# Performance work log

Hardware: AMD Instinct MI355X
Metric: run time of the kernel (lower is better)

## Reference

```python
import jax, jax.numpy as jnp
import numpy as np

B, C, T = 16, 256, 2048          # bsz, z_dim (fsz), tsz
PRED_STEPS, N_NEG, OFFSET = 12, 15, 16
COPIES = 1 + N_NEG


def setup_inputs() -> dict:
    key = jax.random.key(0)
    k1, k2, k3 = jax.random.split(key, 3)
    z = jax.random.normal(k1, (B, C, T), jnp.float32)
    # ConvTranspose2d(C, C, (1, PRED_STEPS)) weight, size-1 kernel-height dim dropped
    weight = jax.random.normal(k2, (C, C, PRED_STEPS), jnp.float32) * 0.02
    bias = jnp.zeros((C,), jnp.float32)
    # negative index sampling (done under no_grad in the original):
    # tszs[k] = k // N_NEG, r in [0, B*T-1), bump by 1 where r >= t
    tszs = jnp.repeat(jnp.arange(T, dtype=jnp.int32), N_NEG)   # (N_NEG*T,)
    r = jax.random.randint(k3, (B, N_NEG * T), 0, B * T - 1, dtype=jnp.int32)
    neg_idxs = r + (r >= tszs[None, :]).astype(jnp.int32)      # values in [0, B*T)
    return {"z": z, "weight": weight, "bias": bias, "neg_idxs": neg_idxs}


def reference(z, weight, bias, neg_idxs):
    # encoder / aggregator are identity: z_hat = z
    # predictor: pred_steps independent linear maps of z_hat
    z_pred = jnp.einsum('bct,coi->boti', z, weight) + bias[None, :, None, None]  # (B,C,T,S)

    # --- sample_negatives: gather from flattened (C, B*T) bank ---
    y = jnp.transpose(z, (1, 0, 2)).reshape(C, B * T)           # (C, B*T)
    negs = y[:, neg_idxs.reshape(-1)]                           # (C, B*N_NEG*T)
    negs = negs.reshape(C, B, N_NEG, T)
    negs = jnp.transpose(negs, (2, 1, 0, 3))                    # (N_NEG, B, C, T)

    targets = jnp.concatenate([z[None], negs], axis=0)          # (COPIES, B, C, T)

    steps = min(PRED_STEPS, T - OFFSET)
    preds = []
    for i in range(steps):  # fixed small structural loop (12 steps)
        off = i + OFFSET
        # ('bct,nbct->tbn') on the overlapping slices, written flat
        p = jnp.einsum('bct,nbct->tbn', z_pred[:, :, :T - off, i], targets[..., off:])
        preds.append(p.reshape(-1))
    predictions = jnp.concatenate(preds).reshape(-1, COPIES)
    labels = jnp.zeros((predictions.shape[0],), dtype=jnp.int32)
    return predictions, labels
```

## Files before the change

### kernel.cpp

```cpp
#include <hip/hip_runtime.h>
#include <hip/hip_bf16.h>

#define B_   16
#define C_   256
#define T_   2048
#define PS   12
#define NNEG 15
#define OFFS 16
#define COPIES 16

#define M_GEMM (B_ * T_)
#define N_GEMM (C_ * PS)
#define K_GEMM C_
#define NPRED 6225408
#define NLAB  389088

using bf16 = __hip_bfloat16;
typedef __attribute__((ext_vector_type(4))) float f32x4;
typedef __attribute__((ext_vector_type(8))) short bf16x8;

__global__ __launch_bounds__(256) void transpose_z(const float* __restrict__ z,
                                                   bf16* __restrict__ zT) {
    __shared__ float tile[32][33];
    int t0 = blockIdx.x * 32, c0 = blockIdx.y * 32, b = blockIdx.z;
    int col = threadIdx.x & 31, r = threadIdx.x >> 5;
    for (int rr = 0; rr < 4; ++rr) {
        int row = r + rr * 8;
        tile[row][col] = z[(size_t)(b * C_ + c0 + row) * T_ + t0 + col];
    }
    __syncthreads();
    for (int rr = 0; rr < 4; ++rr) {
        int row = r + rr * 8;
        zT[(size_t)(b * T_ + t0 + row) * C_ + c0 + col] =
            __float2bfloat16(tile[col][row]);
    }
}

__global__ __launch_bounds__(256) void pack_w(const float* __restrict__ w,
                                              bf16* __restrict__ wTb) {
    int gid = blockIdx.x * 256 + threadIdx.x;
    int j = gid >> 8, c = gid & 255;
    int o = j & 255, i = j >> 8;
    wTb[gid] = __float2bfloat16(w[(size_t)c * (C_ * PS) + o * PS + i]);
}

#define BM 128
#define BN 128
#define BK 64
#define EPAD 136

__global__ __launch_bounds__(256) void gemm_zpred(const bf16* __restrict__ zT,
                                                  const bf16* __restrict__ wTb,
                                                  const float* __restrict__ bias,
                                                  bf16* __restrict__ zp) {
    __shared__ __align__(16) char smem[BM * EPAD * 2];
    bf16* lA = (bf16*)smem;
    bf16* lB = (bf16*)(smem + 16384);
    bf16* lE = (bf16*)smem;

    int bid = (blockIdx.x & 7) * 768 + (blockIdx.x >> 3);
    int bn = bid % (N_GEMM / BN);
    int bm = bid / (N_GEMM / BN);
    int tid = threadIdx.x;
    int wid = tid >> 6, lane = tid & 63;
    int ln15 = lane & 15, kg = lane >> 4;
    int wm = (wid & 1) * 64, wn = (wid >> 1) * 64;
    int row0 = bm * BM, col0 = bn * BN;
    int i_step = col0 >> 8;
    int o0 = col0 & 255;

    f32x4 acc[4][4] = {};

    int rsw = (((lane & 7) ^ ((lane >> 3) & 7)) * 8);
    int srow = wid * 8 + (lane >> 3);
    const bf16* gA0 = zT + (size_t)(row0 + srow) * 256 + rsw;
    const bf16* gB0 = wTb + (size_t)(col0 + srow) * 256 + rsw;

#pragma unroll
    for (int kt = 0; kt < K_GEMM / BK; ++kt) {
        if (kt) __syncthreads();
#pragma unroll
        for (int it = 0; it < 4; ++it) {
            __builtin_amdgcn_global_load_lds(
                (const __attribute__((address_space(1))) void*)(gA0 + it * (size_t)(32 * 256) + kt * BK),
                (__attribute__((address_space(3))) void*)(smem + it * 4096 + wid * 1024), 16, 0, 0);
            __builtin_amdgcn_global_load_lds(
                (const __attribute__((address_space(1))) void*)(gB0 + it * (size_t)(32 * 256) + kt * BK),
                (__attribute__((address_space(3))) void*)(smem + 16384 + it * 4096 + wid * 1024), 16, 0, 0);
        }
        __syncthreads();

#pragma unroll
        for (int kk = 0; kk < 2; ++kk) {
            bf16x8 af[4], bfr[4];
#pragma unroll
            for (int mi = 0; mi < 4; ++mi) {
                int row = wm + mi * 16 + ln15;
                int g = (kk * 4 + kg) ^ (ln15 & 7);
                af[mi] = *(const bf16x8*)&lA[row * BK + g * 8];
            }
#pragma unroll
            for (int ni = 0; ni < 4; ++ni) {
                int row = wn + ni * 16 + ln15;
                int g = (kk * 4 + kg) ^ (ln15 & 7);
                bfr[ni] = *(const bf16x8*)&lB[row * BK + g * 8];
            }
#pragma unroll
            for (int mi = 0; mi < 4; ++mi)
#pragma unroll
                for (int ni = 0; ni < 4; ++ni)
                    acc[mi][ni] = __builtin_amdgcn_mfma_f32_16x16x32_bf16(
                        af[mi], bfr[ni], acc[mi][ni], 0, 0, 0);
        }
    }

    __syncthreads();

    float bv[4];
#pragma unroll
    for (int ni = 0; ni < 4; ++ni) bv[ni] = bias[o0 + wn + ni * 16 + ln15];

#pragma unroll
    for (int mi = 0; mi < 4; ++mi)
#pragma unroll
        for (int ni = 0; ni < 4; ++ni) {
            int col_e = wn + ni * 16 + ln15;
#pragma unroll
            for (int r = 0; r < 4; ++r) {
                int row_e = wm + mi * 16 + kg * 4 + r;
                lE[row_e * EPAD + col_e] = __float2bfloat16(acc[mi][ni][r] + bv[ni]);
            }
        }

    __syncthreads();

#pragma unroll
    for (int e = 0; e < 8; ++e) {
        int row_e = e * 16 + (tid >> 4);
        int grow = row0 + row_e;
        int b = grow >> 11, t = grow & (T_ - 1);
        int s = t + OFFS + i_step;
        if (s < T_) {
            bf16x8 v = *(const bf16x8*)&lE[row_e * EPAD + (tid & 15) * 8];
            *(bf16x8*)(zp + ((size_t)(b * T_ + s) * PS + i_step) * 256 + o0 +
                       (tid & 15) * 8) = v;
        }
    }
}

__global__ __launch_bounds__(256) void predict_kernel(
    const bf16* __restrict__ zT, const bf16* __restrict__ zp,
    const int* __restrict__ neg, float* __restrict__ out) {
    int tid = threadIdx.x;
    int wid = tid >> 6, lane = tid & 63;
    int ln15 = lane & 15, kg = lane >> 4;
    int gw = blockIdx.x * 4 + wid;
    int b = gw / (T_ - OFFS);
    int s = OFFS + gw % (T_ - OFFS);

    int src;
    if (ln15 == 0) src = b * T_ + s;
    else           src = neg[b * (NNEG * T_) + (ln15 - 1) * T_ + s];
    const bf16* arow = zT + (size_t)src * 256 + kg * 8;
    const bf16* brow = zp + ((size_t)(b * T_ + s) * PS + ln15) * 256 + kg * 8;

    f32x4 acc = {0.f, 0.f, 0.f, 0.f};
#pragma unroll
    for (int kk = 0; kk < 8; ++kk) {
        bf16x8 a = *(const bf16x8*)(arow + kk * 32);
        bf16x8 bb = *(const bf16x8*)(brow + kk * 32);
        acc = __builtin_amdgcn_mfma_f32_16x16x32_bf16(a, bb, acc, 0, 0, 0);
    }

    int i = ln15;
    int imax = s - OFFS; if (imax > PS - 1) imax = PS - 1;
    if (i <= imax) {
        int t = s - OFFS - i;
        int base_i = 256 * ((T_ - OFFS) * i - (i * (i - 1)) / 2);
        float* o = out + base_i + (t * B_ + b) * COPIES + kg * 4;
        o[0] = acc[0]; o[1] = acc[1]; o[2] = acc[2]; o[3] = acc[3];
    }
}

extern "C" void kernel_launch(void* const* d_in, const int* in_sizes, int n_in,
                              void* d_out, int out_size, void* d_ws, size_t ws_size,
                              hipStream_t stream) {
    const float* z    = (const float*)d_in[0];
    const float* w    = (const float*)d_in[1];
    const float* bias = (const float*)d_in[2];
    const int*   neg  = (const int*)d_in[3];
    float* out = (float*)d_out;

    char* ws = (char*)d_ws;
    const size_t ZP_BYTES = (size_t)B_ * T_ * PS * 256 * sizeof(bf16);
    bf16* zp  = (bf16*)ws;
    bf16* zT  = (bf16*)(ws + ZP_BYTES + 8192);
    bf16* wTb = (bf16*)(ws + ZP_BYTES + 8192 + (size_t)M_GEMM * 256 * sizeof(bf16));

    transpose_z<<<dim3(T_ / 32, C_ / 32, B_), 256, 0, stream>>>(z, zT);
    pack_w<<<(N_GEMM * 256) / 256, 256, 0, stream>>>(w, wTb);
    gemm_zpred<<<(M_GEMM / BM) * (N_GEMM / BN), 256, 0, stream>>>(zT, wTb, bias, zp);
    predict_kernel<<<(B_ * (T_ - OFFS)) / 4, 256, 0, stream>>>(zT, zp, neg, out);
    hipMemsetAsync(out + NPRED, 0, NLAB * sizeof(float), stream);
}
```

Before: 166.4 us.

## Enlarge GEMM tile to 256x256 with 4-stage async LDS pipeline

```diff
diff --git a/kernel.cpp b/kernel.cpp
--- a/kernel.cpp
+++ b/kernel.cpp
@@ -18,6 +18,12 @@
 using bf16 = __hip_bfloat16;
 typedef __attribute__((ext_vector_type(4))) float f32x4;
 typedef __attribute__((ext_vector_type(8))) short bf16x8;
+
+#define WAITVM(n) asm volatile("s_waitcnt vmcnt(" #n ")" ::: "memory")
+#define GLL(src, dst)                                                        \
+    __builtin_amdgcn_global_load_lds(                                        \
+        (const __attribute__((address_space(1))) void*)(src),                \
+        (__attribute__((address_space(3))) void*)(dst), 16, 0, 0)
 
 __global__ __launch_bounds__(256) void transpose_z(const float* __restrict__ z,
                                                    bf16* __restrict__ zT) {
@@ -44,108 +50,131 @@
     wTb[gid] = __float2bfloat16(w[(size_t)c * (C_ * PS) + o * PS + i]);
 }
 
-#define BM 128
-#define BN 128
-#define BK 64
-#define EPAD 136
-
-__global__ __launch_bounds__(256) void gemm_zpred(const bf16* __restrict__ zT,
-                                                  const bf16* __restrict__ wTb,
-                                                  const float* __restrict__ bias,
-                                                  bf16* __restrict__ zp) {
-    __shared__ __align__(16) char smem[BM * EPAD * 2];
-    bf16* lA = (bf16*)smem;
-    bf16* lB = (bf16*)(smem + 16384);
+#define EPAD 264
+
+__global__ __launch_bounds__(512, 2) void gemm_zpred(
+    const bf16* __restrict__ zT, const bf16* __restrict__ wTb,
+    const float* __restrict__ bias, bf16* __restrict__ zp) {
+    __shared__ __align__(16) char smem[131072];
     bf16* lE = (bf16*)smem;
 
-    int bid = (blockIdx.x & 7) * 768 + (blockIdx.x >> 3);
-    int bn = bid % (N_GEMM / BN);
-    int bm = bid / (N_GEMM / BN);
+    int bid = (blockIdx.x & 7) * 192 + (blockIdx.x >> 3);
+    int bm = bid / (N_GEMM / 256);
+    int bn = bid % (N_GEMM / 256);
+    int row0 = bm * 256;
+    int col0 = bn * 256;
+
     int tid = threadIdx.x;
     int wid = tid >> 6, lane = tid & 63;
     int ln15 = lane & 15, kg = lane >> 4;
-    int wm = (wid & 1) * 64, wn = (wid >> 1) * 64;
-    int row0 = bm * BM, col0 = bn * BN;
-    int i_step = col0 >> 8;
-    int o0 = col0 & 255;
-
-    f32x4 acc[4][4] = {};
-
-    int rsw = (((lane & 7) ^ ((lane >> 3) & 7)) * 8);
-    int srow = wid * 8 + (lane >> 3);
-    const bf16* gA0 = zT + (size_t)(row0 + srow) * 256 + rsw;
-    const bf16* gB0 = wTb + (size_t)(col0 + srow) * 256 + rsw;
-
-#pragma unroll
-    for (int kt = 0; kt < K_GEMM / BK; ++kt) {
-        if (kt) __syncthreads();
-#pragma unroll
-        for (int it = 0; it < 4; ++it) {
-            __builtin_amdgcn_global_load_lds(
-                (const __attribute__((address_space(1))) void*)(gA0 + it * (size_t)(32 * 256) + kt * BK),
-                (__attribute__((address_space(3))) void*)(smem + it * 4096 + wid * 1024), 16, 0, 0);
-            __builtin_amdgcn_global_load_lds(
-                (const __attribute__((address_space(1))) void*)(gB0 + it * (size_t)(32 * 256) + kt * BK),
-                (__attribute__((address_space(3))) void*)(smem + 16384 + it * 4096 + wid * 1024), 16, 0, 0);
+    int wr = wid >> 2, wc = wid & 3;
+
+    int srow = wid * 16 + (lane >> 2);
+    int gsw = ((lane & 3) ^ ((srow >> 1) & 3)) * 8;
+    const bf16* srcA0 = zT + (size_t)(row0 + srow) * 256 + gsw;
+    const bf16* srcA1 = srcA0 + 128 * 256;
+    const bf16* srcB0 = wTb + (size_t)(col0 + srow) * 256 + gsw;
+    const bf16* srcB1 = srcB0 + 128 * 256;
+
+    int offA[8], offB[4];
+#pragma unroll
+    for (int mi = 0; mi < 8; ++mi) {
+        int rl = wr * 128 + mi * 16 + ln15;
+        offA[mi] = (rl >> 7) * 8192 + (rl & 127) * 64 +
+                   ((kg ^ ((rl >> 1) & 3)) * 16);
+    }
+#pragma unroll
+    for (int ni = 0; ni < 4; ++ni) {
+        int cl = wc * 64 + ni * 16 + ln15;
+        offB[ni] = (cl >> 7) * 8192 + (cl & 127) * 64 +
+                   ((kg ^ ((cl >> 1) & 3)) * 16);
+    }
+
+    f32x4 acc[8][4] = {};
+
+#define STAGE(t, slot)                                                       \
+    {                                                                        \
+        const bf16* a0 = srcA0 + (t) * 32;                                   \
+        const bf16* b0 = srcB0 + (t) * 32;                                   \
+        char* d = smem + (slot) * 32768 + wid * 1024;                        \
+        GLL(a0, d);                                                          \
+        GLL(srcA1 + (t) * 32, d + 8192);                                     \
+        GLL(b0, d + 16384);                                                  \
+        GLL(srcB1 + (t) * 32, d + 24576);                                    \
+    }
+
+#define TILE_ITER(KT, VM)                                                    \
+    {                                                                        \
+        WAITVM(VM);                                                          \
+        __builtin_amdgcn_s_barrier();                                        \
+        char* sb = smem + ((KT) & 3) * 32768;                                \
+        bf16x8 af[8], bfr[4];                                                \
+        _Pragma("unroll") for (int mi = 0; mi < 8; ++mi)                     \
+            af[mi] = *(const bf16x8*)(sb + offA[mi]);                        \
+        _Pragma("unroll") for (int ni = 0; ni < 4; ++ni)                     \
+            bfr[ni] = *(const bf16x8*)(sb + 16384 + offB[ni]);               \
+        asm volatile("s_waitcnt lgkmcnt(0)" ::: "memory");                   \
+        __builtin_amdgcn_sched_barrier(0);                                   \
+        __builtin_amdgcn_s_barrier();                                        \
+        if ((KT) + 4 < 8) STAGE((KT) + 4, (KT) & 3);                         \
+        __builtin_amdgcn_s_setprio(1);                                       \
+        _Pragma("unroll") for (int mi = 0; mi < 8; ++mi)                     \
+            _Pragma("unroll") for (int ni = 0; ni < 4; ++ni)                 \
+                acc[mi][ni] = __builtin_amdgcn_mfma_f32_16x16x32_bf16(       \
+                    af[mi], bfr[ni], acc[mi][ni], 0, 0, 0);                  \
+        __builtin_amdgcn_s_setprio(0);                                       \
+    }
+
+    STAGE(0, 0);
+    STAGE(1, 1);
+    STAGE(2, 2);
+    STAGE(3, 3);
+
+    TILE_ITER(0, 12);
+    TILE_ITER(1, 12);
+    TILE_ITER(2, 12);
+    TILE_ITER(3, 12);
+    TILE_ITER(4, 12);
+    TILE_ITER(5, 8);
+    TILE_ITER(6, 4);
+    TILE_ITER(7, 0);
+
+    float bv[4];
+#pragma unroll
+    for (int ni = 0; ni < 4; ++ni) bv[ni] = bias[wc * 64 + ni * 16 + ln15];
+
+    for (int h = 0; h < 2; ++h) {
+        __syncthreads();
+        if (wr == h) {
+#pragma unroll
+            for (int mi = 0; mi < 8; ++mi)
+#pragma unroll
+                for (int ni = 0; ni < 4; ++ni) {
+                    int cl = wc * 64 + ni * 16 + ln15;
+#pragma unroll
+                    for (int r = 0; r < 4; ++r) {
+                        int row_e = mi * 16 + kg * 4 + r;
+                        lE[row_e * EPAD + cl] =
+                            __float2bfloat16(acc[mi][ni][r] + bv[ni]);
+                    }
+                }
         }
         __syncthreads();
-
-#pragma unroll
-        for (int kk = 0; kk < 2; ++kk) {
-            bf16x8 af[4], bfr[4];
-#pragma unroll
-            for (int mi = 0; mi < 4; ++mi) {
-                int row = wm + mi * 16 + ln15;
-                int g = (kk * 4 + kg) ^ (ln15 & 7);
-                af[mi] = *(const bf16x8*)&lA[row * BK + g * 8];
-            }
-#pragma unroll
-            for (int ni = 0; ni < 4; ++ni) {
-                int row = wn + ni * 16 + ln15;
-                int g = (kk * 4 + kg) ^ (ln15 & 7);
-                bfr[ni] = *(const bf16x8*)&lB[row * BK + g * 8];
-            }
-#pragma unroll
-            for (int mi = 0; mi < 4; ++mi)
-#pragma unroll
-                for (int ni = 0; ni < 4; ++ni)
-                    acc[mi][ni] = __builtin_amdgcn_mfma_f32_16x16x32_bf16(
-                        af[mi], bfr[ni], acc[mi][ni], 0, 0, 0);
-        }
-    }
-
-    __syncthreads();
-
-    float bv[4];
-#pragma unroll
-    for (int ni = 0; ni < 4; ++ni) bv[ni] = bias[o0 + wn + ni * 16 + ln15];
-
-#pragma unroll
-    for (int mi = 0; mi < 4; ++mi)
-#pragma unroll
-        for (int ni = 0; ni < 4; ++ni) {
-            int col_e = wn + ni * 16 + ln15;
-#pragma unroll
-            for (int r = 0; r < 4; ++r) {
-                int row_e = wm + mi * 16 + kg * 4 + r;
-                lE[row_e * EPAD + col_e] = __float2bfloat16(acc[mi][ni][r] + bv[ni]);
+#pragma unroll
+        for (int e = 0; e < 8; ++e) {
+            int row_e = e * 16 + (tid >> 5);
+            int grow = row0 + h * 128 + row_e;
+            int b = grow >> 11, t = grow & (T_ - 1);
+            int s = t + OFFS + bn;
+            if (s < T_) {
+                bf16x8 v = *(const bf16x8*)&lE[row_e * EPAD + (tid & 31) * 8];
+                *(bf16x8*)(zp + ((size_t)(b * T_ + s) * PS + bn) * 256 +
+                           (tid & 31) * 8) = v;
             }
         }
-
-    __syncthreads();
-
-#pragma unroll
-    for (int e = 0; e < 8; ++e) {
-        int row_e = e * 16 + (tid >> 4);
-        int grow = row0 + row_e;
-        int b = grow >> 11, t = grow & (T_ - 1);
-        int s = t + OFFS + i_step;
-        if (s < T_) {
-            bf16x8 v = *(const bf16x8*)&lE[row_e * EPAD + (tid & 15) * 8];
-            *(bf16x8*)(zp + ((size_t)(b * T_ + s) * PS + i_step) * 256 + o0 +
-                       (tid & 15) * 8) = v;
-        }
-    }
+    }
+#undef STAGE
+#undef TILE_ITER
 }
 
 __global__ __launch_bounds__(256) void predict_kernel(
@@ -199,7 +228,7 @@
 
     transpose_z<<<dim3(T_ / 32, C_ / 32, B_), 256, 0, stream>>>(z, zT);
     pack_w<<<(N_GEMM * 256) / 256, 256, 0, stream>>>(w, wTb);
-    gemm_zpred<<<(M_GEMM / BM) * (N_GEMM / BN), 256, 0, stream>>>(zT, wTb, bias, zp);
+    gemm_zpred<<<(M_GEMM / 256) * (N_GEMM / 256), 512, 0, stream>>>(zT, wTb, bias, zp);
     predict_kernel<<<(B_ * (T_ - OFFS)) / 4, 256, 0, stream>>>(zT, zp, neg, out);
     hipMemsetAsync(out + NPRED, 0, NLAB * sizeof(float), stream);
 }
```

After: 181.1 us. 1.09x slower.

## Triple-buffer GEMM K-loop with async LDS loads and batch two positions per predict wave

Applied to the files above, without the earlier changes.

```diff
diff --git a/kernel.cpp b/kernel.cpp
--- a/kernel.cpp
+++ b/kernel.cpp
@@ -18,6 +18,12 @@
 using bf16 = __hip_bfloat16;
 typedef __attribute__((ext_vector_type(4))) float f32x4;
 typedef __attribute__((ext_vector_type(8))) short bf16x8;
+
+#define WAITVM(n) asm volatile("s_waitcnt vmcnt(" #n ")" ::: "memory")
+#define GLL(src, dst)                                                        \
+    __builtin_amdgcn_global_load_lds(                                        \
+        (const __attribute__((address_space(1))) void*)(src),                \
+        (__attribute__((address_space(3))) void*)(dst), 16, 0, 0)
 
 __global__ __launch_bounds__(256) void transpose_z(const float* __restrict__ z,
                                                    bf16* __restrict__ zT) {
@@ -44,75 +50,87 @@
     wTb[gid] = __float2bfloat16(w[(size_t)c * (C_ * PS) + o * PS + i]);
 }
 
-#define BM 128
-#define BN 128
-#define BK 64
 #define EPAD 136
 
 __global__ __launch_bounds__(256) void gemm_zpred(const bf16* __restrict__ zT,
                                                   const bf16* __restrict__ wTb,
                                                   const float* __restrict__ bias,
                                                   bf16* __restrict__ zp) {
-    __shared__ __align__(16) char smem[BM * EPAD * 2];
-    bf16* lA = (bf16*)smem;
-    bf16* lB = (bf16*)(smem + 16384);
+    __shared__ __align__(16) char smem[49152];
     bf16* lE = (bf16*)smem;
 
     int bid = (blockIdx.x & 7) * 768 + (blockIdx.x >> 3);
-    int bn = bid % (N_GEMM / BN);
-    int bm = bid / (N_GEMM / BN);
+    int bn = bid % (N_GEMM / 128);
+    int bm = bid / (N_GEMM / 128);
     int tid = threadIdx.x;
     int wid = tid >> 6, lane = tid & 63;
     int ln15 = lane & 15, kg = lane >> 4;
     int wm = (wid & 1) * 64, wn = (wid >> 1) * 64;
-    int row0 = bm * BM, col0 = bn * BN;
+    int row0 = bm * 128, col0 = bn * 128;
     int i_step = col0 >> 8;
     int o0 = col0 & 255;
 
+    int gsw = ((lane & 3) ^ ((lane >> 3) & 3)) * 8;
+    int srow = wid * 16 + (lane >> 2);
+    const bf16* srcA = zT + (size_t)(row0 + srow) * 256 + gsw;
+    const bf16* srcB = wTb + (size_t)(col0 + srow) * 256 + gsw;
+
+    int offA[4], offB[4];
+#pragma unroll
+    for (int mi = 0; mi < 4; ++mi) {
+        int r = wm + mi * 16 + ln15;
+        offA[mi] = r * 64 + ((kg ^ ((r >> 1) & 3)) * 16);
+    }
+#pragma unroll
+    for (int ni = 0; ni < 4; ++ni) {
+        int c = wn + ni * 16 + ln15;
+        offB[ni] = 8192 + c * 64 + ((kg ^ ((c >> 1) & 3)) * 16);
+    }
+
     f32x4 acc[4][4] = {};
 
-    int rsw = (((lane & 7) ^ ((lane >> 3) & 7)) * 8);
-    int srow = wid * 8 + (lane >> 3);
-    const bf16* gA0 = zT + (size_t)(row0 + srow) * 256 + rsw;
-    const bf16* gB0 = wTb + (size_t)(col0 + srow) * 256 + rsw;
-
-#pragma unroll
-    for (int kt = 0; kt < K_GEMM / BK; ++kt) {
-        if (kt) __syncthreads();
-#pragma unroll
-        for (int it = 0; it < 4; ++it) {
-            __builtin_amdgcn_global_load_lds(
-                (const __attribute__((address_space(1))) void*)(gA0 + it * (size_t)(32 * 256) + kt * BK),
-                (__attribute__((address_space(3))) void*)(smem + it * 4096 + wid * 1024), 16, 0, 0);
-            __builtin_amdgcn_global_load_lds(
-                (const __attribute__((address_space(1))) void*)(gB0 + it * (size_t)(32 * 256) + kt * BK),
-                (__attribute__((address_space(3))) void*)(smem + 16384 + it * 4096 + wid * 1024), 16, 0, 0);
-        }
-        __syncthreads();
-
-#pragma unroll
-        for (int kk = 0; kk < 2; ++kk) {
-            bf16x8 af[4], bfr[4];
-#pragma unroll
-            for (int mi = 0; mi < 4; ++mi) {
-                int row = wm + mi * 16 + ln15;
-                int g = (kk * 4 + kg) ^ (ln15 & 7);
-                af[mi] = *(const bf16x8*)&lA[row * BK + g * 8];
-            }
-#pragma unroll
-            for (int ni = 0; ni < 4; ++ni) {
-                int row = wn + ni * 16 + ln15;
-                int g = (kk * 4 + kg) ^ (ln15 & 7);
-                bfr[ni] = *(const bf16x8*)&lB[row * BK + g * 8];
-            }
-#pragma unroll
-            for (int mi = 0; mi < 4; ++mi)
-#pragma unroll
-                for (int ni = 0; ni < 4; ++ni)
-                    acc[mi][ni] = __builtin_amdgcn_mfma_f32_16x16x32_bf16(
-                        af[mi], bfr[ni], acc[mi][ni], 0, 0, 0);
-        }
-    }
+#define STAGE(t, slot_base)                                                  \
+    {                                                                        \
+        char* d = smem + (slot_base) + wid * 1024;                           \
+        const bf16* sa = srcA + (t) * 32;                                    \
+        const bf16* sb2 = srcB + (t) * 32;                                   \
+        GLL(sa, d);                                                          \
+        GLL(sa + 64 * 256, d + 4096);                                        \
+        GLL(sb2, d + 8192);                                                  \
+        GLL(sb2 + 64 * 256, d + 12288);                                      \
+    }
+
+#define TILE_BODY(slot_base, VMN)                                            \
+    {                                                                        \
+        WAITVM(VMN);                                                         \
+        __builtin_amdgcn_s_barrier();                                        \
+        const char* sb = smem + (slot_base);                                 \
+        bf16x8 af[4], bfr[4];                                                \
+        _Pragma("unroll") for (int mi = 0; mi < 4; ++mi)                     \
+            af[mi] = *(const bf16x8*)(sb + offA[mi]);                        \
+        _Pragma("unroll") for (int ni = 0; ni < 4; ++ni)                     \
+            bfr[ni] = *(const bf16x8*)(sb + offB[ni]);                       \
+        asm volatile("s_waitcnt lgkmcnt(0)" ::: "memory");                   \
+        __builtin_amdgcn_sched_barrier(0);                                   \
+        __builtin_amdgcn_s_barrier();                                        \
+        __builtin_amdgcn_s_setprio(1);                                       \
+        _Pragma("unroll") for (int mi = 0; mi < 4; ++mi)                     \
+            _Pragma("unroll") for (int ni = 0; ni < 4; ++ni)                 \
+                acc[mi][ni] = __builtin_amdgcn_mfma_f32_16x16x32_bf16(       \
+                    af[mi], bfr[ni], acc[mi][ni], 0, 0, 0);                  \
+        __builtin_amdgcn_s_setprio(0);                                       \
+    }
+
+    STAGE(0, 0);
+    STAGE(1, 16384);
+    STAGE(2, 32768);  TILE_BODY(0, 8);
+    STAGE(3, 0);      TILE_BODY(16384, 8);
+    STAGE(4, 16384);  TILE_BODY(32768, 8);
+    STAGE(5, 32768);  TILE_BODY(0, 8);
+    STAGE(6, 0);      TILE_BODY(16384, 8);
+    STAGE(7, 16384);  TILE_BODY(32768, 8);
+                      TILE_BODY(0, 4);
+                      TILE_BODY(16384, 0);
 
     __syncthreads();
 
@@ -146,6 +164,8 @@
                        (tid & 15) * 8) = v;
         }
     }
+#undef STAGE
+#undef TILE_BODY
 }
 
 __global__ __launch_bounds__(256) void predict_kernel(
@@ -154,31 +174,50 @@
     int tid = threadIdx.x;
     int wid = tid >> 6, lane = tid & 63;
     int ln15 = lane & 15, kg = lane >> 4;
-    int gw = blockIdx.x * 4 + wid;
+    int gw = (blockIdx.x * 4 + wid) * 2;
     int b = gw / (T_ - OFFS);
     int s = OFFS + gw % (T_ - OFFS);
 
-    int src;
-    if (ln15 == 0) src = b * T_ + s;
-    else           src = neg[b * (NNEG * T_) + (ln15 - 1) * T_ + s];
-    const bf16* arow = zT + (size_t)src * 256 + kg * 8;
-    const bf16* brow = zp + ((size_t)(b * T_ + s) * PS + ln15) * 256 + kg * 8;
-
-    f32x4 acc = {0.f, 0.f, 0.f, 0.f};
+    int src0, src1;
+    if (ln15 == 0) {
+        src0 = b * T_ + s;
+        src1 = src0 + 1;
+    } else {
+        const int* np = neg + b * (NNEG * T_) + (ln15 - 1) * T_ + s;
+        src0 = np[0];
+        src1 = np[1];
+    }
+    const bf16* a0 = zT + (size_t)src0 * 256 + kg * 8;
+    const bf16* a1 = zT + (size_t)src1 * 256 + kg * 8;
+    const bf16* b0 = zp + ((size_t)(b * T_ + s) * PS + ln15) * 256 + kg * 8;
+    const bf16* b1 = b0 + PS * 256;
+
+    f32x4 acc0 = {0.f, 0.f, 0.f, 0.f};
+    f32x4 acc1 = {0.f, 0.f, 0.f, 0.f};
 #pragma unroll
     for (int kk = 0; kk < 8; ++kk) {
-        bf16x8 a = *(const bf16x8*)(arow + kk * 32);
-        bf16x8 bb = *(const bf16x8*)(brow + kk * 32);
-        acc = __builtin_amdgcn_mfma_f32_16x16x32_bf16(a, bb, acc, 0, 0, 0);
+        bf16x8 av0 = *(const bf16x8*)(a0 + kk * 32);
+        bf16x8 bv0 = *(const bf16x8*)(b0 + kk * 32);
+        bf16x8 av1 = *(const bf16x8*)(a1 + kk * 32);
+        bf16x8 bv1 = *(const bf16x8*)(b1 + kk * 32);
+        acc0 = __builtin_amdgcn_mfma_f32_16x16x32_bf16(av0, bv0, acc0, 0, 0, 0);
+        acc1 = __builtin_amdgcn_mfma_f32_16x16x32_bf16(av1, bv1, acc1, 0, 0, 0);
     }
 
     int i = ln15;
-    int imax = s - OFFS; if (imax > PS - 1) imax = PS - 1;
-    if (i <= imax) {
-        int t = s - OFFS - i;
-        int base_i = 256 * ((T_ - OFFS) * i - (i * (i - 1)) / 2);
-        float* o = out + base_i + (t * B_ + b) * COPIES + kg * 4;
-        o[0] = acc[0]; o[1] = acc[1]; o[2] = acc[2]; o[3] = acc[3];
+    if (i < PS) {
+#pragma unroll 2
+        for (int p = 0; p < 2; ++p) {
+            int sp = s + p;
+            int imax = sp - OFFS;
+            if (i <= imax) {
+                int t = sp - OFFS - i;
+                int base_i = 256 * ((T_ - OFFS) * i - (i * (i - 1)) / 2);
+                float* o = out + base_i + (t * B_ + b) * COPIES + kg * 4;
+                f32x4 a = p ? acc1 : acc0;
+                o[0] = a[0]; o[1] = a[1]; o[2] = a[2]; o[3] = a[3];
+            }
+        }
     }
 }
 
@@ -199,7 +238,7 @@
 
     transpose_z<<<dim3(T_ / 32, C_ / 32, B_), 256, 0, stream>>>(z, zT);
     pack_w<<<(N_GEMM * 256) / 256, 256, 0, stream>>>(w, wTb);
-    gemm_zpred<<<(M_GEMM / BM) * (N_GEMM / BN), 256, 0, stream>>>(zT, wTb, bias, zp);
-    predict_kernel<<<(B_ * (T_ - OFFS)) / 4, 256, 0, stream>>>(zT, zp, neg, out);
+    gemm_zpred<<<(M_GEMM / 128) * (N_GEMM / 128), 256, 0, stream>>>(zT, wTb, bias, zp);
+    predict_kernel<<<(B_ * (T_ - OFFS)) / 8, 256, 0, stream>>>(zT, zp, neg, out);
     hipMemsetAsync(out + NPRED, 0, NLAB * sizeof(float), stream);
 }
```

New measurement: 159.9 us. 1.04x faster.

## Fuse predictor GEMM and prediction dot-products into one kernel

Applied to the files above, without the earlier changes.

```diff
diff --git a/kernel.cpp b/kernel.cpp
--- a/kernel.cpp
+++ b/kernel.cpp
@@ -8,16 +8,17 @@
 #define NNEG 15
 #define OFFS 16
 #define COPIES 16
-
-#define M_GEMM (B_ * T_)
-#define N_GEMM (C_ * PS)
-#define K_GEMM C_
 #define NPRED 6225408
 #define NLAB  389088
 
 using bf16 = __hip_bfloat16;
 typedef __attribute__((ext_vector_type(4))) float f32x4;
 typedef __attribute__((ext_vector_type(8))) short bf16x8;
+
+#define GLL(src, dst)                                                        \
+    __builtin_amdgcn_global_load_lds(                                        \
+        (const __attribute__((address_space(1))) void*)(src),                \
+        (__attribute__((address_space(3))) void*)(dst), 16, 0, 0)
 
 __global__ __launch_bounds__(256) void transpose_z(const float* __restrict__ z,
                                                    bf16* __restrict__ zT) {
@@ -44,141 +45,155 @@
     wTb[gid] = __float2bfloat16(w[(size_t)c * (C_ * PS) + o * PS + i]);
 }
 
-#define BM 128
-#define BN 128
-#define BK 64
-#define EPAD 136
-
-__global__ __launch_bounds__(256) void gemm_zpred(const bf16* __restrict__ zT,
-                                                  const bf16* __restrict__ wTb,
-                                                  const float* __restrict__ bias,
-                                                  bf16* __restrict__ zp) {
-    __shared__ __align__(16) char smem[BM * EPAD * 2];
-    bf16* lA = (bf16*)smem;
-    bf16* lB = (bf16*)(smem + 16384);
-    bf16* lE = (bf16*)smem;
-
-    int bid = (blockIdx.x & 7) * 768 + (blockIdx.x >> 3);
-    int bn = bid % (N_GEMM / BN);
-    int bm = bid / (N_GEMM / BN);
-    int tid = threadIdx.x;
-    int wid = tid >> 6, lane = tid & 63;
-    int ln15 = lane & 15, kg = lane >> 4;
-    int wm = (wid & 1) * 64, wn = (wid >> 1) * 64;
-    int row0 = bm * BM, col0 = bn * BN;
-    int i_step = col0 >> 8;
-    int o0 = col0 & 255;
-
-    f32x4 acc[4][4] = {};
-
-    int rsw = (((lane & 7) ^ ((lane >> 3) & 7)) * 8);
-    int srow = wid * 8 + (lane >> 3);
-    const bf16* gA0 = zT + (size_t)(row0 + srow) * 256 + rsw;
-    const bf16* gB0 = wTb + (size_t)(col0 + srow) * 256 + rsw;
-
-#pragma unroll
-    for (int kt = 0; kt < K_GEMM / BK; ++kt) {
-        if (kt) __syncthreads();
-#pragma unroll
-        for (int it = 0; it < 4; ++it) {
-            __builtin_amdgcn_global_load_lds(
-                (const __attribute__((address_space(1))) void*)(gA0 + it * (size_t)(32 * 256) + kt * BK),
-                (__attribute__((address_space(3))) void*)(smem + it * 4096 + wid * 1024), 16, 0, 0);
-            __builtin_amdgcn_global_load_lds(
-                (const __attribute__((address_space(1))) void*)(gB0 + it * (size_t)(32 * 256) + kt * BK),
-                (__attribute__((address_space(3))) void*)(smem + 16384 + it * 4096 + wid * 1024), 16, 0, 0);
-        }
+__global__ __launch_bounds__(512, 2) void fused_kernel(
+    const bf16* __restrict__ zT, const bf16* __restrict__ wTb,
+    const float* __restrict__ bias, const int* __restrict__ neg,
+    float* __restrict__ out) {
+    __shared__ __align__(16) char smem[103424];
+    char* smA = smem;
+    char* smZ = smem + 40960;
+    float* smBias = (float*)(smem + 102400);
+
+    const int tid = threadIdx.x;
+    const int wid = tid >> 6, lane = tid & 63;
+    const int ln15 = lane & 15, kg = lane >> 4;
+
+    int raw = blockIdx.x;
+    int bid = (raw & 7) * 64 + (raw >> 3);
+    const int b = bid >> 5, sblk = bid & 31;
+    const int s0 = OFFS + sblk * 64;
+    const int t_base = s0 - 27;
+
+    if (tid < C_) smBias[tid] = bias[tid];
+
+    {
+        int g31 = lane & 31;
+#pragma unroll
+        for (int g = 0; g < 5; ++g) {
+            int r2 = wid * 10 + g * 2;
+            int rt = r2 + (lane >> 5);
+            int t = t_base + rt;
+            t = t < 0 ? 0 : (t > T_ - 1 ? T_ - 1 : t);
+            const char* src = (const char*)(zT + (size_t)(b * T_ + t) * C_) +
+                              ((g31 ^ (rt & 7)) << 4);
+            GLL(src, smA + r2 * 512);
+        }
+    }
+    asm volatile("s_waitcnt vmcnt(0)" ::: "memory");
+    __syncthreads();
+
+    const int s_w = s0 + wid * 8;
+    const int s_rd = s_w > T_ - 8 ? T_ - 8 : s_w;
+    int srcrow[8];
+    if (lane == 0) {
+#pragma unroll
+        for (int it = 0; it < 8; ++it) srcrow[it] = b * T_ + s_rd + it;
+    } else if (lane < 16) {
+        const int* np = neg + b * (NNEG * T_) + (lane - 1) * T_ + s_rd;
+        int4 n0 = *(const int4*)np;
+        int4 n1 = *(const int4*)(np + 4);
+        srcrow[0] = n0.x; srcrow[1] = n0.y; srcrow[2] = n0.z; srcrow[3] = n0.w;
+        srcrow[4] = n1.x; srcrow[5] = n1.y; srcrow[6] = n1.z; srcrow[7] = n1.w;
+    } else {
+#pragma unroll
+        for (int it = 0; it < 8; ++it) srcrow[it] = 0;
+    }
+
+    const int wn = wid * 48;
+    int wrow[3];
+#pragma unroll
+    for (int j = 0; j < 3; ++j) {
+        int col = wn + j * 16 + ln15;
+        wrow[j] = (col >> 5) * 256 + (col & 31);
+    }
+    int abase[5], a7[5];
+#pragma unroll
+    for (int m = 0; m < 5; ++m) {
+        int r = m * 16 + ln15;
+        abase[m] = r * 512;
+        a7[m] = r & 7;
+    }
+    const int ii = ln15 < PS ? ln15 : 0;
+
+    f32x4 oacc[8] = {};
+
+#pragma unroll 1
+    for (int cs = 0; cs < 8; ++cs) {
+        f32x4 acc[5][3] = {};
+#pragma unroll
+        for (int k = 0; k < 8; ++k) {
+            bf16x8 bfr[3];
+#pragma unroll
+            for (int j = 0; j < 3; ++j)
+                bfr[j] = *(const bf16x8*)((const char*)wTb +
+                          (((size_t)(wrow[j] + cs * 32)) << 9) +
+                          (k << 6) + (kg << 4));
+            bf16x8 af[5];
+#pragma unroll
+            for (int m = 0; m < 5; ++m)
+                af[m] = *(const bf16x8*)(smA + abase[m] +
+                                         (((k * 4 + kg) ^ a7[m]) << 4));
+#pragma unroll
+            for (int m = 0; m < 5; ++m)
+#pragma unroll
+                for (int j = 0; j < 3; ++j)
+                    acc[m][j] = __builtin_amdgcn_mfma_f32_16x16x32_bf16(
+                        af[m], bfr[j], acc[m][j], 0, 0, 0);
+        }
+
         __syncthreads();
 
-#pragma unroll
-        for (int kk = 0; kk < 2; ++kk) {
-            bf16x8 af[4], bfr[4];
-#pragma unroll
-            for (int mi = 0; mi < 4; ++mi) {
-                int row = wm + mi * 16 + ln15;
-                int g = (kk * 4 + kg) ^ (ln15 & 7);
-                af[mi] = *(const bf16x8*)&lA[row * BK + g * 8];
+        {
+            float bv0 = smBias[cs * 32 + ln15];
+            float bv1 = smBias[cs * 32 + 16 + ln15];
+#pragma unroll
+            for (int m = 0; m < 5; ++m)
+#pragma unroll
+                for (int j = 0; j < 3; ++j) {
+                    int col = wn + j * 16 + ln15;
+                    float bvj = (((wid & 1) + j) & 1) ? bv1 : bv0;
+#pragma unroll
+                    for (int r = 0; r < 4; ++r) {
+                        int row = m * 16 + kg * 4 + r;
+                        int gz = (col >> 3) ^ (row & 7);
+                        *(bf16*)(smZ + row * 768 + (gz << 4) +
+                                 ((col & 7) << 1)) =
+                            __float2bfloat16(acc[m][j][r] + bvj);
+                    }
+                }
+        }
+
+        __syncthreads();
+
+        {
+            bf16x8 t8[8], zf[8];
+#pragma unroll
+            for (int it = 0; it < 8; ++it) {
+                int row = __shfl(srcrow[it], ln15);
+                t8[it] = *(const bf16x8*)((const char*)zT +
+                          ((size_t)row << 9) + (cs << 6) + (kg << 4));
+                int rowP = wid * 8 + it + 11 - ii;
+                zf[it] = *(const bf16x8*)(smZ + rowP * 768 +
+                          (((ii * 4 + kg) ^ (rowP & 7)) << 4));
             }
 #pragma unroll
-            for (int ni = 0; ni < 4; ++ni) {
-                int row = wn + ni * 16 + ln15;
-                int g = (kk * 4 + kg) ^ (ln15 & 7);
-                bfr[ni] = *(const bf16x8*)&lB[row * BK + g * 8];
+            for (int it = 0; it < 8; ++it)
+                oacc[it] = __builtin_amdgcn_mfma_f32_16x16x32_bf16(
+                    t8[it], zf[it], oacc[it], 0, 0, 0);
+        }
+    }
+
+    if (ln15 < PS) {
+        int i = ln15;
+        int bi = 256 * ((T_ - OFFS) * i - (i * (i - 1)) / 2);
+#pragma unroll
+        for (int it = 0; it < 8; ++it) {
+            int s = s_w + it;
+            if (s < T_ && i <= s - OFFS) {
+                int t = s - OFFS - i;
+                *(f32x4*)(out + bi + (t * B_ + b) * COPIES + kg * 4) = oacc[it];
             }
-#pragma unroll
-            for (int mi = 0; mi < 4; ++mi)
-#pragma unroll
-                for (int ni = 0; ni < 4; ++ni)
-                    acc[mi][ni] = __builtin_amdgcn_mfma_f32_16x16x32_bf16(
-                        af[mi], bfr[ni], acc[mi][ni], 0, 0, 0);
-        }
-    }
-
-    __syncthreads();
-
-    float bv[4];
-#pragma unroll
-    for (int ni = 0; ni < 4; ++ni) bv[ni] = bias[o0 + wn + ni * 16 + ln15];
-
-#pragma unroll
-    for (int mi = 0; mi < 4; ++mi)
-#pragma unroll
-        for (int ni = 0; ni < 4; ++ni) {
-            int col_e = wn + ni * 16 + ln15;
-#pragma unroll
-            for (int r = 0; r < 4; ++r) {
-                int row_e = wm + mi * 16 + kg * 4 + r;
-                lE[row_e * EPAD + col_e] = __float2bfloat16(acc[mi][ni][r] + bv[ni]);
-            }
-        }
-
-    __syncthreads();
-
-#pragma unroll
-    for (int e = 0; e < 8; ++e) {
-        int row_e = e * 16 + (tid >> 4);
-        int grow = row0 + row_e;
-        int b = grow >> 11, t = grow & (T_ - 1);
-        int s = t + OFFS + i_step;
-        if (s < T_) {
-            bf16x8 v = *(const bf16x8*)&lE[row_e * EPAD + (tid & 15) * 8];
-            *(bf16x8*)(zp + ((size_t)(b * T_ + s) * PS + i_step) * 256 + o0 +
-                       (tid & 15) * 8) = v;
-        }
-    }
-}
-
-__global__ __launch_bounds__(256) void predict_kernel(
-    const bf16* __restrict__ zT, const bf16* __restrict__ zp,
-    const int* __restrict__ neg, float* __restrict__ out) {
-    int tid = threadIdx.x;
-    int wid = tid >> 6, lane = tid & 63;
-    int ln15 = lane & 15, kg = lane >> 4;
-    int gw = blockIdx.x * 4 + wid;
-    int b = gw / (T_ - OFFS);
-    int s = OFFS + gw % (T_ - OFFS);
-
-    int src;
-    if (ln15 == 0) src = b * T_ + s;
-    else           src = neg[b * (NNEG * T_) + (ln15 - 1) * T_ + s];
-    const bf16* arow = zT + (size_t)src * 256 + kg * 8;
-    const bf16* brow = zp + ((size_t)(b * T_ + s) * PS + ln15) * 256 + kg * 8;
-
-    f32x4 acc = {0.f, 0.f, 0.f, 0.f};
-#pragma unroll
-    for (int kk = 0; kk < 8; ++kk) {
-        bf16x8 a = *(const bf16x8*)(arow + kk * 32);
-        bf16x8 bb = *(const bf16x8*)(brow + kk * 32);
-        acc = __builtin_amdgcn_mfma_f32_16x16x32_bf16(a, bb, acc, 0, 0, 0);
-    }
-
-    int i = ln15;
-    int imax = s - OFFS; if (imax > PS - 1) imax = PS - 1;
-    if (i <= imax) {
-        int t = s - OFFS - i;
-        int base_i = 256 * ((T_ - OFFS) * i - (i * (i - 1)) / 2);
-        float* o = out + base_i + (t * B_ + b) * COPIES + kg * 4;
-        o[0] = acc[0]; o[1] = acc[1]; o[2] = acc[2]; o[3] = acc[3];
+        }
     }
 }
 
@@ -192,14 +207,11 @@
     float* out = (float*)d_out;
 
     char* ws = (char*)d_ws;
-    const size_t ZP_BYTES = (size_t)B_ * T_ * PS * 256 * sizeof(bf16);
-    bf16* zp  = (bf16*)ws;
-    bf16* zT  = (bf16*)(ws + ZP_BYTES + 8192);
-    bf16* wTb = (bf16*)(ws + ZP_BYTES + 8192 + (size_t)M_GEMM * 256 * sizeof(bf16));
+    bf16* zT  = (bf16*)ws;
+    bf16* wTb = (bf16*)(ws + (size_t)B_ * T_ * C_ * sizeof(bf16));
 
     transpose_z<<<dim3(T_ / 32, C_ / 32, B_), 256, 0, stream>>>(z, zT);
-    pack_w<<<(N_GEMM * 256) / 256, 256, 0, stream>>>(w, wTb);
-    gemm_zpred<<<(M_GEMM / BM) * (N_GEMM / BN), 256, 0, stream>>>(zT, wTb, bias, zp);
-    predict_kernel<<<(B_ * (T_ - OFFS)) / 4, 256, 0, stream>>>(zT, zp, neg, out);
+    pack_w<<<(C_ * PS * C_) / 256, 256, 0, stream>>>(w, wTb);
+    fused_kernel<<<512, 512, 0, stream>>>(zT, wTb, bias, neg, out);
     hipMemsetAsync(out + NPRED, 0, NLAB * sizeof(float), stream);
 }
```

Result: slower. 175.2 us (+5.3%).
